# Optimization experiments

Measured on AMD Instinct MI355X. Metric: run time of the kernel, lower is better.

Reference implementation:

```python
import jax, jax.numpy as jnp
import numpy as np

B, N, D, E = 256, 192, 512, 1024
H = E // 2          # MLP hidden = 512
K = 58              # round(0.3 * 192), hardcoded in the torch forward
EPS_L2 = 1e-8
EPS_BN = 1e-5


def setup_inputs() -> dict:
    key = jax.random.key(0)
    ks = jax.random.split(key, 8)
    s = 0.02
    return {
        "all_patch_embeddings": jax.random.normal(ks[0], (B, N, D), dtype=jnp.float32),
        "attention_map": jax.random.uniform(ks[1], (B, N + 1, N + 1), dtype=jnp.float32),
        # fc: Linear(D, E)
        "W_fc": jax.random.normal(ks[2], (E, D), dtype=jnp.float32) * s,
        "b_fc": jnp.zeros((E,), dtype=jnp.float32),
        # mlp layer 0: Linear(D, H) + BatchNorm1d(H) + ReLU
        "W1": jax.random.normal(ks[3], (H, D), dtype=jnp.float32) * s,
        "b1": jnp.zeros((H,), dtype=jnp.float32),
        "gamma1": jnp.ones((H,), dtype=jnp.float32),
        "beta1": jnp.zeros((H,), dtype=jnp.float32),
        # mlp layer 1: Linear(H, E) (no BN/ReLU applied on last layer)
        "W2": jax.random.normal(ks[4], (E, H), dtype=jnp.float32) * s,
        "b2": jnp.zeros((E,), dtype=jnp.float32),
    }


def reference(all_patch_embeddings, attention_map, W_fc, b_fc, W1, b1, gamma1, beta1, W2, b2):
    # CLS-row attention over the 192 patch tokens: [B, N]
    cls_attn = attention_map[:, 0, 1:]
    # torch.sort(descending)[...,:K] == top-k indices (batched, replaces python loop)
    _, idx = jax.lax.top_k(cls_attn, K)                      # [B, K] int32
    # batched gather replacing the per-sample index_select loop
    sel = jnp.take_along_axis(all_patch_embeddings, idx[:, :, None], axis=1)  # [B, K, D]
    # l2norm over last dim
    norm = jnp.sqrt(jnp.sum(sel * sel, axis=-1, keepdims=True)) + EPS_L2
    base = sel / norm
    # .half() cast in the original (round-trip to fp16 precision)
    base = base.astype(jnp.float16).astype(jnp.float32)
    # fc branch
    feat_fc = jnp.einsum('bkd,ed->bke', base, W_fc) + b_fc    # [B, K, E]
    # mlp branch (num_layers=2): Linear -> BN(train-mode batch stats) -> ReLU -> Linear
    h = jnp.einsum('bkd,hd->bkh', base, W1) + b1              # [B, K, H]
    hf = h.reshape(B * K, H)
    mu = jnp.mean(hf, axis=0)
    var = jnp.var(hf, axis=0)
    hf = (hf - mu) * jax.lax.rsqrt(var + EPS_BN) * gamma1 + beta1
    h = jax.nn.relu(hf).reshape(B, K, H)
    feat_mlp = jnp.einsum('bkh,eh->bke', h, W2) + b2          # [B, K, E]
    feats = feat_mlp + feat_fc
    # maxk_pool1d_var with k=1 and lengths == K reduces to max over token dim
    return jnp.max(feats, axis=1).astype(jnp.float32)         # [B, E]
```

## Files before the change

### kernel.cpp

```cpp
#include <hip/hip_runtime.h>
#include <hip/hip_fp16.h>

#define B_ 256
#define N_ 192
#define D_ 512
#define E_ 1024
#define H_ 512
#define K_ 58
#define M_ (B_*K_)
#define M2_ (B_*64)

typedef _Float16 f16;
typedef unsigned int u32;
typedef _Float16 half8 __attribute__((ext_vector_type(8)));
typedef float floatx16 __attribute__((ext_vector_type(16)));

__device__ inline half8 cvt8(float4 f0, float4 f1) {
  half8 r;
  r[0]=(f16)f0.x; r[1]=(f16)f0.y; r[2]=(f16)f0.z; r[3]=(f16)f0.w;
  r[4]=(f16)f1.x; r[5]=(f16)f1.y; r[6]=(f16)f1.z; r[7]=(f16)f1.w;
  return r;
}

__device__ inline void gl_lds16(const f16* g, f16* l) {
  __builtin_amdgcn_global_load_lds((const __attribute__((address_space(1))) u32*)g,
                                   (__attribute__((address_space(3))) u32*)l, 16, 0, 0);
}

__device__ inline void stage128(const f16* gbase, int gstride, f16* sT, int w, int lane) {
  int lrow  = lane >> 2;
  int chunk = (lane & 3) ^ ((lane >> 3) & 3);
  gl_lds16(gbase + (size_t)(w*16      + lrow)*gstride + chunk*8, &sT[(w*16)*32]);
  gl_lds16(gbase + (size_t)(64 + w*16 + lrow)*gstride + chunk*8, &sT[(64 + w*16)*32]);
}

__global__ void setup_kernel(const float* __restrict__ Wfc, const float* __restrict__ W2,
                             const float* __restrict__ W1, const float* __restrict__ attn,
                             const float* __restrict__ emb,
                             f16* __restrict__ Wcat, f16* __restrict__ W1_16,
                             f16* __restrict__ A16, float* __restrict__ csum) {
  __shared__ float sv[N_];
  __shared__ int sidx[K_];
  __shared__ int cnt;
  int blk = blockIdx.x, t = threadIdx.x;
  if (blk < 512) {
    int idx = (blk*256 + t)*8;
    int e = idx >> 10, c = idx & 1023;
    const float* src = (c < 512) ? (Wfc + (size_t)e*512 + c)
                                 : (W2  + (size_t)e*512 + (c-512));
    half8 o = cvt8(((const float4*)src)[0], ((const float4*)src)[1]);
    *(uint4*)(Wcat + idx) = *(uint4*)&o;
  } else if (blk < 640) {
    int idx = ((blk-512)*256 + t)*8;
    const float* src = W1 + idx;
    half8 o = cvt8(((const float4*)src)[0], ((const float4*)src)[1]);
    *(uint4*)(W1_16 + idx) = *(uint4*)&o;
  } else if (blk < 896) {
    int b = blk - 640;
    if (t == 0) cnt = 0;
    if (t < N_) sv[t] = attn[(size_t)b*193*193 + 1 + t];
    __syncthreads();
    if (t < N_) {
      float v = sv[t]; int rank = 0;
      for (int j = 0; j < N_; ++j) {
        float vj = sv[j];
        rank += (vj > v) || (vj == v && j < t);
      }
      if (rank < K_) sidx[atomicAdd(&cnt, 1)] = t;
    }
    __syncthreads();
    int w = t >> 6, lane = t & 63;
    for (int slot = w; slot < 64; slot += 4) {
      f16* dst = A16 + ((size_t)b*64 + slot)*1024 + lane*8;
      if (slot < K_) {
        const float* src = emb + ((size_t)b*N_ + sidx[slot])*D_ + lane*8;
        float4 v0 = ((const float4*)src)[0];
        float4 v1 = ((const float4*)src)[1];
        float s = v0.x*v0.x + v0.y*v0.y + v0.z*v0.z + v0.w*v0.w
                + v1.x*v1.x + v1.y*v1.y + v1.z*v1.z + v1.w*v1.w;
        #pragma unroll
        for (int off = 32; off > 0; off >>= 1) s += __shfl_xor(s, off);
        float inv = 1.0f / (sqrtf(s) + 1e-8f);
        half8 o;
        o[0]=(f16)(v0.x*inv); o[1]=(f16)(v0.y*inv); o[2]=(f16)(v0.z*inv); o[3]=(f16)(v0.w*inv);
        o[4]=(f16)(v1.x*inv); o[5]=(f16)(v1.y*inv); o[6]=(f16)(v1.z*inv); o[7]=(f16)(v1.w*inv);
        *(uint4*)dst = *(uint4*)&o;
      } else {
        uint4 z; z.x=0u; z.y=0u; z.z=0u; z.w=0u;
        *(uint4*)dst = z;
      }
    }
  } else {
    float4 z; z.x=0.f; z.y=0.f; z.z=0.f; z.w=0.f;
    ((float4*)csum)[t] = z;
  }
}

__launch_bounds__(256, 2)
__global__ void gemm1_kernel(const f16* __restrict__ A16, const f16* __restrict__ W1_16,
                             const float* __restrict__ b1, f16* __restrict__ Aout,
                             float* __restrict__ csum, float* __restrict__ css) {
  __shared__ f16 sA[2][128*32];
  __shared__ f16 sB[2][128*32];
  __shared__ float sSum[4][64], sSS[4][64];
  int t = threadIdx.x;
  int g = blockIdx.x;
  int xcd = g & 7, rest = g >> 3;
  int n0 = (rest & 3) * 128;
  int m0 = (xcd + 8*(rest >> 2)) * 128;
  int lane = t & 63, w = t >> 6;
  int l31 = lane & 31, khalf = lane >> 5, swz = (l31 >> 1) & 3;
  int rw = w & 1, cw = w >> 1;
  floatx16 acc[2][2] = {};
  const f16* Ab = A16 + (size_t)m0*1024;
  const f16* Bb = W1_16 + (size_t)n0*512;
  stage128(Ab, 1024, sA[0], w, lane);
  stage128(Bb, 512,  sB[0], w, lane);
  __syncthreads();
  for (int it = 0; it < 16; ++it) {
    int cur = it & 1, nxt = cur ^ 1;
    if (it < 15) {
      stage128(Ab + (it+1)*32, 1024, sA[nxt], w, lane);
      stage128(Bb + (it+1)*32, 512,  sB[nxt], w, lane);
    }
    #pragma unroll
    for (int s = 0; s < 2; ++s) {
      int ko = ((s*2 + khalf) ^ swz) * 8;
      half8 a[2], bf[2];
      #pragma unroll
      for (int i = 0; i < 2; ++i) a[i]  = *(const half8*)&sA[cur][(rw*64 + i*32 + l31)*32 + ko];
      #pragma unroll
      for (int j = 0; j < 2; ++j) bf[j] = *(const half8*)&sB[cur][(cw*64 + j*32 + l31)*32 + ko];
      #pragma unroll
      for (int i = 0; i < 2; ++i)
        #pragma unroll
        for (int j = 0; j < 2; ++j)
          acc[i][j] = __builtin_amdgcn_mfma_f32_32x32x16_f16(a[i], bf[j], acc[i][j], 0, 0, 0);
    }
    __syncthreads();
  }
  #pragma unroll
  for (int jt = 0; jt < 2; ++jt) {
    int col = n0 + cw*64 + jt*32 + l31;
    float bias = b1[col];
    float s = 0.f, ss = 0.f;
    #pragma unroll
    for (int i = 0; i < 2; ++i) {
      #pragma unroll
      for (int rg = 0; rg < 16; ++rg) {
        int rib = i*32 + (rg&3) + 8*(rg>>2) + 4*khalf;
        float x = acc[i][jt][rg] + bias;
        Aout[(size_t)(m0 + rw*64 + rib)*1024 + 512 + col] = (f16)x;
        if (i == 0 || rib < K_) { s += x; ss += x*x; }
      }
    }
    s  += __shfl_xor(s, 32);
    ss += __shfl_xor(ss, 32);
    if (lane < 32) { sSum[w][jt*32 + l31] = s; sSS[w][jt*32 + l31] = ss; }
  }
  __syncthreads();
  if (t < 128) {
    int c = t;
    int w0 = 2*(c >> 6), ci = c & 63;
    atomicAdd(&csum[n0 + c], sSum[w0][ci] + sSum[w0+1][ci]);
    atomicAdd(&css[n0 + c],  sSS[w0][ci]  + sSS[w0+1][ci]);
  }
}

__launch_bounds__(256, 3)
__global__ void fused_kernel(const f16* __restrict__ A16, const f16* __restrict__ Wcat,
                             const float* __restrict__ csum, const float* __restrict__ css,
                             const float* __restrict__ gamma, const float* __restrict__ beta,
                             const float* __restrict__ bfc, const float* __restrict__ b2,
                             float* __restrict__ out) {
  __shared__ f16 sA[2][128*32];
  __shared__ f16 sB[2][128*32];
  __shared__ float sSc[H_], sSh[H_];
  __shared__ float sMax[4][64];
  int t = threadIdx.x;
  int g = blockIdx.x;
  int xcd = g & 7, rest = g >> 3;
  int e0 = (rest & 7) * 128;
  int bm = xcd + 8*(rest >> 3);
  int lane = t & 63, w = t >> 6;
  int l31 = lane & 31, khalf = lane >> 5, swz = (l31 >> 1) & 3;
  int rw = w & 1, cw = w >> 1;
  #pragma unroll
  for (int jj = 0; jj < 2; ++jj) {
    int j = t + jj*256;
    float mu  = csum[j] * (1.0f/M_);
    float var = css[j] * (1.0f/M_) - mu*mu;
    float sc  = gamma[j] * rsqrtf(var + 1e-5f);
    sSc[j] = sc;
    sSh[j] = beta[j] - mu*sc;
  }
  floatx16 acc[2][2] = {};
  const f16* Ab = A16 + (size_t)bm*128*1024;
  const f16* Bb = Wcat + (size_t)e0*1024;
  int rr = t >> 2;
  int rslot  = (t & 3) * 8;
  int rchunk = (t & 3) ^ ((t >> 3) & 3);
  bool pad = (rr >= K_);
  stage128(Ab, 1024, sA[0], w, lane);
  stage128(Bb, 1024, sB[0], w, lane);
  __syncthreads();
  for (int it = 0; it < 32; ++it) {
    int cur = it & 1, nxt = cur ^ 1;
    int kn = (it + 1) * 32;
    uint4 h0, h1;
    bool regp = false;
    if (it < 31) {
      stage128(Bb + kn, 1024, sB[nxt], w, lane);
      if (kn < 512) {
        stage128(Ab + kn, 1024, sA[nxt], w, lane);
      } else {
        regp = true;
        const f16* hp = Ab + (size_t)rr*1024 + kn + rchunk*8;
        h0 = *(const uint4*)hp;
        h1 = *(const uint4*)(hp + (size_t)64*1024);
      }
    }
    #pragma unroll
    for (int s = 0; s < 2; ++s) {
      int ko = ((s*2 + khalf) ^ swz) * 8;
      half8 a[2], bf[2];
      #pragma unroll
      for (int i = 0; i < 2; ++i) a[i]  = *(const half8*)&sA[cur][(rw*64 + i*32 + l31)*32 + ko];
      #pragma unroll
      for (int j = 0; j < 2; ++j) bf[j] = *(const half8*)&sB[cur][(cw*64 + j*32 + l31)*32 + ko];
      #pragma unroll
      for (int i = 0; i < 2; ++i)
        #pragma unroll
        for (int j = 0; j < 2; ++j)
          acc[i][j] = __builtin_amdgcn_mfma_f32_32x32x16_f16(a[i], bf[j], acc[i][j], 0, 0, 0);
    }
    if (regp) {
      int cb = kn - 512 + rchunk*8;
      float4 sc0 = *(float4*)&sSc[cb], sc1 = *(float4*)&sSc[cb+4];
      float4 sh0 = *(float4*)&sSh[cb], sh1 = *(float4*)&sSh[cb+4];
      half8 v0 = *(half8*)&h0, v1 = *(half8*)&h1;
      half8 o0, o1;
      o0[0]=(f16)fmaxf((float)v0[0]*sc0.x+sh0.x, 0.f);
      o0[1]=(f16)fmaxf((float)v0[1]*sc0.y+sh0.y, 0.f);
      o0[2]=(f16)fmaxf((float)v0[2]*sc0.z+sh0.z, 0.f);
      o0[3]=(f16)fmaxf((float)v0[3]*sc0.w+sh0.w, 0.f);
      o0[4]=(f16)fmaxf((float)v0[4]*sc1.x+sh1.x, 0.f);
      o0[5]=(f16)fmaxf((float)v0[5]*sc1.y+sh1.y, 0.f);
      o0[6]=(f16)fmaxf((float)v0[6]*sc1.z+sh1.z, 0.f);
      o0[7]=(f16)fmaxf((float)v0[7]*sc1.w+sh1.w, 0.f);
      o1[0]=(f16)fmaxf((float)v1[0]*sc0.x+sh0.x, 0.f);
      o1[1]=(f16)fmaxf((float)v1[1]*sc0.y+sh0.y, 0.f);
      o1[2]=(f16)fmaxf((float)v1[2]*sc0.z+sh0.z, 0.f);
      o1[3]=(f16)fmaxf((float)v1[3]*sc0.w+sh0.w, 0.f);
      o1[4]=(f16)fmaxf((float)v1[4]*sc1.x+sh1.x, 0.f);
      o1[5]=(f16)fmaxf((float)v1[5]*sc1.y+sh1.y, 0.f);
      o1[6]=(f16)fmaxf((float)v1[6]*sc1.z+sh1.z, 0.f);
      o1[7]=(f16)fmaxf((float)v1[7]*sc1.w+sh1.w, 0.f);
      if (pad) {
        uint4 z; z.x=0u; z.y=0u; z.z=0u; z.w=0u;
        *(uint4*)&o0 = z; *(uint4*)&o1 = z;
      }
      *(uint4*)&sA[nxt][rr*32 + rslot]        = *(uint4*)&o0;
      *(uint4*)&sA[nxt][(64 + rr)*32 + rslot] = *(uint4*)&o1;
    }
    __syncthreads();
  }
  #pragma unroll
  for (int jt = 0; jt < 2; ++jt) {
    float mx = -3.0e38f;
    #pragma unroll
    for (int i = 0; i < 2; ++i) {
      #pragma unroll
      for (int rg = 0; rg < 16; ++rg) {
        int rib = i*32 + (rg&3) + 8*(rg>>2) + 4*khalf;
        if (i == 0 || rib < K_) mx = fmaxf(mx, acc[i][jt][rg]);
      }
    }
    mx = fmaxf(mx, __shfl_xor(mx, 32));
    if (lane < 32) sMax[w][jt*32 + l31] = mx;
  }
  __syncthreads();
  #pragma unroll
  for (int bb = 0; bb < 2; ++bb) {
    int c = t & 127;
    if ((t >> 7) == bb) {
      float mx = sMax[bb + 2*(c >> 6)][c & 63];
      int e = e0 + c;
      out[((size_t)bm*2 + bb)*E_ + e] = mx + bfc[e] + b2[e];
    }
  }
}

extern "C" void kernel_launch(void* const* d_in, const int* in_sizes, int n_in,
                              void* d_out, int out_size, void* d_ws, size_t ws_size,
                              hipStream_t stream) {
  const float* emb   = (const float*)d_in[0];
  const float* attn  = (const float*)d_in[1];
  const float* Wfc   = (const float*)d_in[2];
  const float* bfc   = (const float*)d_in[3];
  const float* W1    = (const float*)d_in[4];
  const float* b1    = (const float*)d_in[5];
  const float* gamma = (const float*)d_in[6];
  const float* beta  = (const float*)d_in[7];
  const float* W2    = (const float*)d_in[8];
  const float* b2    = (const float*)d_in[9];
  float* out = (float*)d_out;

  char* ws = (char*)d_ws;
  f16*   A16   = (f16*)(ws);
  f16*   Wcat  = (f16*)(ws + 33554432);
  f16*   W1_16 = (f16*)(ws + 35651584);
  float* csum  = (float*)(ws + 36175872);
  float* css   = (float*)(ws + 36177920);

  setup_kernel<<<897, 256, 0, stream>>>(Wfc, W2, W1, attn, emb, Wcat, W1_16, A16, csum);
  gemm1_kernel<<<512, 256, 0, stream>>>(A16, W1_16, b1, A16, csum, css);
  fused_kernel<<<1024, 256, 0, stream>>>(A16, Wcat, csum, css, gamma, beta, bfc, b2, out);
}
```

Before: 238.1 us.

## Triple-buffer LDS staging with manual vmcnt waits in both GEMM kernels

Both GEMM kernels move from double-buffered LDS with a full __syncthreads per k-step to a three-stage ring buffer. Global-to-LDS loads are issued two tiles ahead, and each step waits only on partial vmcnt before a raw barrier. In the fused kernel, the register-prefetched hidden activations are now normalized and written one step later, so their global latency is hidden too. The cost is more LDS per block (about 52KB), which may limit occupancy against the launch bounds of 2 and 3 blocks per CU. The hand-written waitcnt logic is also fragile.

Measured after the change: 248.0 us. +4.2%, slower.

```diff
diff --git a/kernel.cpp b/kernel.cpp
--- a/kernel.cpp
+++ b/kernel.cpp
@@ -14,6 +14,27 @@
 typedef unsigned int u32;
 typedef _Float16 half8 __attribute__((ext_vector_type(8)));
 typedef float floatx16 __attribute__((ext_vector_type(16)));
+
+#define WAIT_VMCNT4() asm volatile("s_waitcnt vmcnt(4)" ::: "memory")
+#define WAIT_VMCNT0() asm volatile("s_waitcnt vmcnt(0)" ::: "memory")
+#define WAIT_LGKM0()  asm volatile("s_waitcnt lgkmcnt(0)" ::: "memory")
+#define BAR()         __builtin_amdgcn_s_barrier()
+#define FENCE()       __builtin_amdgcn_sched_barrier(0)
+
+#define COMPUTE_STEP(pA, pB) do {                                              \
+    _Pragma("unroll")                                                          \
+    for (int s_ = 0; s_ < 2; ++s_) {                                           \
+      int ko_ = ((s_*2 + khalf) ^ swz) * 8;                                    \
+      half8 a0_ = *(const half8*)&(pA)[(rw*64 +      l31)*32 + ko_];           \
+      half8 a1_ = *(const half8*)&(pA)[(rw*64 + 32 + l31)*32 + ko_];           \
+      half8 b0_ = *(const half8*)&(pB)[(cw*64 +      l31)*32 + ko_];           \
+      half8 b1_ = *(const half8*)&(pB)[(cw*64 + 32 + l31)*32 + ko_];           \
+      acc[0][0] = __builtin_amdgcn_mfma_f32_32x32x16_f16(a0_, b0_, acc[0][0], 0,0,0); \
+      acc[0][1] = __builtin_amdgcn_mfma_f32_32x32x16_f16(a0_, b1_, acc[0][1], 0,0,0); \
+      acc[1][0] = __builtin_amdgcn_mfma_f32_32x32x16_f16(a1_, b0_, acc[1][0], 0,0,0); \
+      acc[1][1] = __builtin_amdgcn_mfma_f32_32x32x16_f16(a1_, b1_, acc[1][1], 0,0,0); \
+    }                                                                          \
+  } while (0)
 
 __device__ inline half8 cvt8(float4 f0, float4 f1) {
   half8 r;
@@ -100,9 +121,11 @@
 __global__ void gemm1_kernel(const f16* __restrict__ A16, const f16* __restrict__ W1_16,
                              const float* __restrict__ b1, f16* __restrict__ Aout,
                              float* __restrict__ csum, float* __restrict__ css) {
-  __shared__ f16 sA[2][128*32];
-  __shared__ f16 sB[2][128*32];
-  __shared__ float sSum[4][64], sSS[4][64];
+  __shared__ __align__(16) char smem[51200];
+  f16* sAb = (f16*)smem;
+  f16* sBb = (f16*)(smem + 24576);
+  float (*sSum)[64] = (float(*)[64])(smem + 49152);
+  float (*sSS)[64]  = (float(*)[64])(smem + 50176);
   int t = threadIdx.x;
   int g = blockIdx.x;
   int xcd = g & 7, rest = g >> 3;
@@ -114,30 +137,28 @@
   floatx16 acc[2][2] = {};
   const f16* Ab = A16 + (size_t)m0*1024;
   const f16* Bb = W1_16 + (size_t)n0*512;
-  stage128(Ab, 1024, sA[0], w, lane);
-  stage128(Bb, 512,  sB[0], w, lane);
-  __syncthreads();
-  for (int it = 0; it < 16; ++it) {
-    int cur = it & 1, nxt = cur ^ 1;
-    if (it < 15) {
-      stage128(Ab + (it+1)*32, 1024, sA[nxt], w, lane);
-      stage128(Bb + (it+1)*32, 512,  sB[nxt], w, lane);
-    }
-    #pragma unroll
-    for (int s = 0; s < 2; ++s) {
-      int ko = ((s*2 + khalf) ^ swz) * 8;
-      half8 a[2], bf[2];
-      #pragma unroll
-      for (int i = 0; i < 2; ++i) a[i]  = *(const half8*)&sA[cur][(rw*64 + i*32 + l31)*32 + ko];
-      #pragma unroll
-      for (int j = 0; j < 2; ++j) bf[j] = *(const half8*)&sB[cur][(cw*64 + j*32 + l31)*32 + ko];
-      #pragma unroll
-      for (int i = 0; i < 2; ++i)
-        #pragma unroll
-        for (int j = 0; j < 2; ++j)
-          acc[i][j] = __builtin_amdgcn_mfma_f32_32x32x16_f16(a[i], bf[j], acc[i][j], 0, 0, 0);
-    }
-    __syncthreads();
+  stage128(Ab,      1024, sAb,        w, lane);
+  stage128(Bb,      512,  sBb,        w, lane);
+  stage128(Ab + 32, 1024, sAb + 4096, w, lane);
+  stage128(Bb + 32, 512,  sBb + 4096, w, lane);
+  int c0 = 0;
+  #pragma unroll 1
+  for (int i = 0; i < 14; ++i) {
+    WAIT_VMCNT4(); WAIT_LGKM0(); BAR(); FENCE();
+    int bS = c0 + 2; if (bS >= 3) bS -= 3;
+    int kn = (i + 2) * 32;
+    stage128(Ab + kn, 1024, sAb + bS*4096, w, lane);
+    stage128(Bb + kn, 512,  sBb + bS*4096, w, lane);
+    COMPUTE_STEP(sAb + c0*4096, sBb + c0*4096);
+    c0 = c0 + 1; if (c0 >= 3) c0 -= 3;
+  }
+  {
+    WAIT_VMCNT4(); WAIT_LGKM0(); BAR(); FENCE();
+    COMPUTE_STEP(sAb + 2*4096, sBb + 2*4096);
+  }
+  {
+    WAIT_VMCNT0(); WAIT_LGKM0(); BAR(); FENCE();
+    COMPUTE_STEP(sAb, sBb);
   }
   #pragma unroll
   for (int jt = 0; jt < 2; ++jt) {
@@ -173,10 +194,12 @@
                              const float* __restrict__ gamma, const float* __restrict__ beta,
                              const float* __restrict__ bfc, const float* __restrict__ b2,
                              float* __restrict__ out) {
-  __shared__ f16 sA[2][128*32];
-  __shared__ f16 sB[2][128*32];
-  __shared__ float sSc[H_], sSh[H_];
-  __shared__ float sMax[4][64];
+  __shared__ __align__(16) char smem[53248];
+  f16* sAb = (f16*)smem;
+  f16* sBb = (f16*)(smem + 24576);
+  float* sSc = (float*)(smem + 49152);
+  float* sSh = (float*)(smem + 51200);
+  float (*sMax)[64] = (float(*)[64])(smem + 49152);
   int t = threadIdx.x;
   int g = blockIdx.x;
   int xcd = g & 7, rest = g >> 3;
@@ -201,44 +224,33 @@
   int rslot  = (t & 3) * 8;
   int rchunk = (t & 3) ^ ((t >> 3) & 3);
   bool pad = (rr >= K_);
-  stage128(Ab, 1024, sA[0], w, lane);
-  stage128(Bb, 1024, sB[0], w, lane);
-  __syncthreads();
-  for (int it = 0; it < 32; ++it) {
-    int cur = it & 1, nxt = cur ^ 1;
-    int kn = (it + 1) * 32;
-    uint4 h0, h1;
-    bool regp = false;
-    if (it < 31) {
-      stage128(Bb + kn, 1024, sB[nxt], w, lane);
-      if (kn < 512) {
-        stage128(Ab + kn, 1024, sA[nxt], w, lane);
-      } else {
-        regp = true;
-        const f16* hp = Ab + (size_t)rr*1024 + kn + rchunk*8;
-        h0 = *(const uint4*)hp;
-        h1 = *(const uint4*)(hp + (size_t)64*1024);
-      }
-    }
-    #pragma unroll
-    for (int s = 0; s < 2; ++s) {
-      int ko = ((s*2 + khalf) ^ swz) * 8;
-      half8 a[2], bf[2];
-      #pragma unroll
-      for (int i = 0; i < 2; ++i) a[i]  = *(const half8*)&sA[cur][(rw*64 + i*32 + l31)*32 + ko];
-      #pragma unroll
-      for (int j = 0; j < 2; ++j) bf[j] = *(const half8*)&sB[cur][(cw*64 + j*32 + l31)*32 + ko];
-      #pragma unroll
-      for (int i = 0; i < 2; ++i)
-        #pragma unroll
-        for (int j = 0; j < 2; ++j)
-          acc[i][j] = __builtin_amdgcn_mfma_f32_32x32x16_f16(a[i], bf[j], acc[i][j], 0, 0, 0);
-    }
-    if (regp) {
-      int cb = kn - 512 + rchunk*8;
+  uint4 hp0 = {}, hp1 = {};
+  stage128(Ab,      1024, sAb,        w, lane);
+  stage128(Bb,      1024, sBb,        w, lane);
+  stage128(Ab + 32, 1024, sAb + 4096, w, lane);
+  stage128(Bb + 32, 1024, sBb + 4096, w, lane);
+  int c0 = 0;
+  #pragma unroll 1
+  for (int i = 0; i < 30; ++i) {
+    WAIT_VMCNT4(); WAIT_LGKM0(); BAR(); FENCE();
+    int bW = c0 + 1; if (bW >= 3) bW -= 3;
+    int bS = c0 + 2; if (bS >= 3) bS -= 3;
+    int tn = i + 2, kn = tn * 32;
+    uint4 hc0, hc1;
+    if (tn < 16) {
+      stage128(Ab + kn, 1024, sAb + bS*4096, w, lane);
+    } else {
+      const f16* hp = Ab + (size_t)rr*1024 + kn + rchunk*8;
+      hc0 = *(const uint4*)hp;
+      hc1 = *(const uint4*)(hp + (size_t)64*1024);
+    }
+    stage128(Bb + kn, 1024, sBb + bS*4096, w, lane);
+    COMPUTE_STEP(sAb + c0*4096, sBb + c0*4096);
+    if (i >= 15) {
+      int cb = (i + 1)*32 - 512 + rchunk*8;
       float4 sc0 = *(float4*)&sSc[cb], sc1 = *(float4*)&sSc[cb+4];
       float4 sh0 = *(float4*)&sSh[cb], sh1 = *(float4*)&sSh[cb+4];
-      half8 v0 = *(half8*)&h0, v1 = *(half8*)&h1;
+      half8 v0 = *(half8*)&hp0, v1 = *(half8*)&hp1;
       half8 o0, o1;
       o0[0]=(f16)fmaxf((float)v0[0]*sc0.x+sh0.x, 0.f);
       o0[1]=(f16)fmaxf((float)v0[1]*sc0.y+sh0.y, 0.f);
@@ -260,11 +272,48 @@
         uint4 z; z.x=0u; z.y=0u; z.z=0u; z.w=0u;
         *(uint4*)&o0 = z; *(uint4*)&o1 = z;
       }
-      *(uint4*)&sA[nxt][rr*32 + rslot]        = *(uint4*)&o0;
-      *(uint4*)&sA[nxt][(64 + rr)*32 + rslot] = *(uint4*)&o1;
-    }
-    __syncthreads();
-  }
+      *(uint4*)&sAb[bW*4096 + rr*32 + rslot]        = *(uint4*)&o0;
+      *(uint4*)&sAb[bW*4096 + (64 + rr)*32 + rslot] = *(uint4*)&o1;
+    }
+    hp0 = hc0; hp1 = hc1;
+    c0 = bW;
+  }
+  {
+    WAIT_VMCNT4(); WAIT_LGKM0(); BAR(); FENCE();
+    COMPUTE_STEP(sAb, sBb);
+    int cb = 31*32 - 512 + rchunk*8;
+    float4 sc0 = *(float4*)&sSc[cb], sc1 = *(float4*)&sSc[cb+4];
+    float4 sh0 = *(float4*)&sSh[cb], sh1 = *(float4*)&sSh[cb+4];
+    half8 v0 = *(half8*)&hp0, v1 = *(half8*)&hp1;
+    half8 o0, o1;
+    o0[0]=(f16)fmaxf((float)v0[0]*sc0.x+sh0.x, 0.f);
+    o0[1]=(f16)fmaxf((float)v0[1]*sc0.y+sh0.y, 0.f);
+    o0[2]=(f16)fmaxf((float)v0[2]*sc0.z+sh0.z, 0.f);
+    o0[3]=(f16)fmaxf((float)v0[3]*sc0.w+sh0.w, 0.f);
+    o0[4]=(f16)fmaxf((float)v0[4]*sc1.x+sh1.x, 0.f);
+    o0[5]=(f16)fmaxf((float)v0[5]*sc1.y+sh1.y, 0.f);
+    o0[6]=(f16)fmaxf((float)v0[6]*sc1.z+sh1.z, 0.f);
+    o0[7]=(f16)fmaxf((float)v0[7]*sc1.w+sh1.w, 0.f);
+    o1[0]=(f16)fmaxf((float)v1[0]*sc0.x+sh0.x, 0.f);
+    o1[1]=(f16)fmaxf((float)v1[1]*sc0.y+sh0.y, 0.f);
+    o1[2]=(f16)fmaxf((float)v1[2]*sc0.z+sh0.z, 0.f);
+    o1[3]=(f16)fmaxf((float)v1[3]*sc0.w+sh0.w, 0.f);
+    o1[4]=(f16)fmaxf((float)v1[4]*sc1.x+sh1.x, 0.f);
+    o1[5]=(f16)fmaxf((float)v1[5]*sc1.y+sh1.y, 0.f);
+    o1[6]=(f16)fmaxf((float)v1[6]*sc1.z+sh1.z, 0.f);
+    o1[7]=(f16)fmaxf((float)v1[7]*sc1.w+sh1.w, 0.f);
+    if (pad) {
+      uint4 z; z.x=0u; z.y=0u; z.z=0u; z.w=0u;
+      *(uint4*)&o0 = z; *(uint4*)&o1 = z;
+    }
+    *(uint4*)&sAb[1*4096 + rr*32 + rslot]        = *(uint4*)&o0;
+    *(uint4*)&sAb[1*4096 + (64 + rr)*32 + rslot] = *(uint4*)&o1;
+  }
+  {
+    WAIT_VMCNT0(); WAIT_LGKM0(); BAR(); FENCE();
+    COMPUTE_STEP(sAb + 4096, sBb + 4096);
+  }
+  __syncthreads();
   #pragma unroll
   for (int jt = 0; jt < 2; ++jt) {
     float mx = -3.0e38f;
```
